# Optimization experiments

Measured on AMD Instinct MI355X. Metric: run time of the kernel, lower is better.

The kernel has to match this reference:

```python
import math
import jax, jax.numpy as jnp
import numpy as np

HEADS = 8


def setup_inputs() -> dict:
    key = jax.random.key(0)
    k1, k2, k3 = jax.random.split(key, 3)
    bs, C, H, Wd = 16, 512, 32, 32
    x = jax.random.normal(k1, (bs, C, H, Wd), dtype=jnp.float32)
    pos_enc = jax.random.normal(k2, (bs, C, H, Wd), dtype=jnp.float32)
    # 1x1 conv: weight [3C, C], bias [3C]
    W = jax.random.normal(k3, (3 * C, C), dtype=jnp.float32) * (1.0 / math.sqrt(C))
    b = jnp.zeros((3 * C,), dtype=jnp.float32)
    return {"x": x, "pos_enc": pos_enc, "W": W, "b": b}


def reference(x, pos_enc, W, b):
    x = x + pos_enc
    bs, C, H, Wd = x.shape
    heads = HEADS
    dim = C // heads
    N = H * Wd
    # 1x1 conv == channel matmul
    c = jnp.einsum('oc,bchw->bohw', W, x) + b[None, :, None, None]
    c = c.reshape(bs, 3, heads, dim, N)
    q = c[:, 0]  # [bs, heads, dim, N]
    k = c[:, 1]
    v = c[:, 2]
    scale = 1.0 / math.sqrt(dim)
    attn = jnp.einsum('bhdn,bhdm->bhnm', q, k) * scale  # [bs, heads, N, N]
    attn = jax.nn.softmax(attn, axis=-1)
    out = jnp.einsum('bhdm,bhnm->bhdn', v, attn)  # [bs, heads, dim, N]
    return x + out.reshape(bs, C, H, Wd)
```

## Files before the change

### kernel.cpp

```cpp
#include <hip/hip_runtime.h>
#include <stdint.h>


typedef __attribute__((ext_vector_type(4))) float f32x4;
typedef __attribute__((ext_vector_type(8))) __bf16 bf16x8;
typedef __attribute__((ext_vector_type(8))) short short8;
typedef __attribute__((ext_vector_type(4))) short short4v;

#define DEVINL static __device__ __forceinline__

DEVINL unsigned short f2bf(float f) {
  unsigned u = __builtin_bit_cast(unsigned, f);
  u += 0x7FFFu + ((u >> 16) & 1u);
  return (unsigned short)(u >> 16);
}

DEVINL void gload16(const void* g, const void* lds) {
  __builtin_amdgcn_global_load_lds(
      (const __attribute__((address_space(1))) unsigned int*)(uintptr_t)g,
      (__attribute__((address_space(3))) unsigned int*)(uintptr_t)lds, 16, 0, 0);
}

template <int CTRL>
DEVINL float dppmax(float x) {
  int yi = __builtin_amdgcn_update_dpp(0, __builtin_bit_cast(int, x), CTRL, 0xF, 0xF, true);
  return fmaxf(x, __builtin_bit_cast(float, yi));
}
DEVINL float rowmax16(float x) {
  x = dppmax<0xB1>(x);
  x = dppmax<0x4E>(x);
  x = dppmax<0x141>(x);
  x = dppmax<0x140>(x);
  return x;
}

__global__ __launch_bounds__(256) void k_conv(const float* __restrict__ Wf,
                                              unsigned short* __restrict__ wbo) {
  const int i = (blockIdx.x * 256 + threadIdx.x) * 4;
  const f32x4 v = *(const f32x4*)(Wf + i);
  short4v t;
  t[0] = (short)f2bf(v[0]); t[1] = (short)f2bf(v[1]);
  t[2] = (short)f2bf(v[2]); t[3] = (short)f2bf(v[3]);
  *(short4v*)(wbo + i) = t;
}

__global__ __launch_bounds__(256) void k_addt(const float* __restrict__ x,
                                              const float* __restrict__ pe,
                                              float* __restrict__ out,
                                              unsigned short* __restrict__ st) {
  __shared__ unsigned short T[64][64];
  const int b = blockIdx.z, ct = blockIdx.y, nt = blockIdx.x;
  const int tid = threadIdx.x;
  const int cl = tid >> 4, n4 = (tid & 15) * 4;
  const size_t base = ((size_t)b * 512 + ct * 64) * 1024 + nt * 64;
#pragma unroll
  for (int i = 0; i < 4; ++i) {
    const int c = cl + i * 16;
    const size_t idx = base + (size_t)c * 1024 + n4;
    const f32x4 xv = *(const f32x4*)(x + idx);
    const f32x4 pv = *(const f32x4*)(pe + idx);
    const f32x4 s = xv + pv;
    *(f32x4*)(out + idx) = s;
    short4v t;
    t[0] = (short)f2bf(s[0]); t[1] = (short)f2bf(s[1]);
    t[2] = (short)f2bf(s[2]); t[3] = (short)f2bf(s[3]);
    *(short4v*)&T[c][n4] = t;
  }
  __syncthreads();
  const int nl = tid >> 2, cq = tid & 3;
  short8 v0, v1;
#pragma unroll
  for (int j = 0; j < 8; ++j) {
    v0[j] = (short)T[cq * 16 + j][nl];
    v1[j] = (short)T[cq * 16 + 8 + j][nl];
  }
  const size_t so = ((size_t)b * 1024 + nt * 64 + nl) * 512 + ct * 64 + cq * 16;
  *(short8*)(st + so) = v0;
  *(short8*)(st + so + 8) = v1;
}

__global__ __launch_bounds__(256, 2) void k_gemm(const unsigned short* __restrict__ st,
                                                 const unsigned short* __restrict__ wb,
                                                 const float* __restrict__ bias,
                                                 unsigned short* __restrict__ qb,
                                                 unsigned short* __restrict__ kb,
                                                 unsigned short* __restrict__ vb) {
  const int b = blockIdx.z;
  const int mode = (blockIdx.y >= 8);
  const int tile_m = (mode ? (blockIdx.y - 8) : blockIdx.y) * 128;
  const int tile_n = blockIdx.x * 128;
  const unsigned short* Ag;
  const unsigned short* Bg;
  if (!mode) {
    Ag = st + (size_t)b * 524288 + (size_t)tile_m * 512;
    Bg = wb + (size_t)tile_n * 512;
  } else {
    Ag = wb + (size_t)(1024 + tile_m) * 512;
    Bg = st + (size_t)b * 524288 + (size_t)tile_n * 512;
  }
  __shared__ unsigned short As[4096];
  __shared__ unsigned short Bs[4096];
  const int tid = threadIdx.x, lane = tid & 63, w = tid >> 6;
  const int wrow = w >> 1, wcol = w & 1, lr = lane & 15, g = lane >> 4;
  f32x4 acc[4][4] = {};
  for (int kt = 0; kt < 16; ++kt) {
    __syncthreads();
#pragma unroll
    for (int j = 0; j < 2; ++j) {
      const int D = j * 4096 + w * 1024 + lane * 16;
      const int row = D >> 6, off = D & 63;
      gload16((const char*)Ag + (size_t)row * 1024 + kt * 64 + off,
              (const char*)As + j * 4096 + w * 1024);
      gload16((const char*)Bg + (size_t)row * 1024 + kt * 64 + off,
              (const char*)Bs + j * 4096 + w * 1024);
    }
    __syncthreads();
    bf16x8 a[4], bb[4];
#pragma unroll
    for (int i = 0; i < 4; ++i) {
      a[i]  = *(const bf16x8*)(As + (wrow * 64 + i * 16 + lr) * 32 + g * 8);
      bb[i] = *(const bf16x8*)(Bs + (wcol * 64 + i * 16 + lr) * 32 + g * 8);
    }
#pragma unroll
    for (int i = 0; i < 4; ++i)
#pragma unroll
      for (int jj = 0; jj < 4; ++jj)
        acc[i][jj] = __builtin_amdgcn_mfma_f32_16x16x32_bf16(a[i], bb[jj], acc[i][jj], 0, 0, 0);
  }
  if (!mode) {
#pragma unroll
    for (int jj = 0; jj < 4; ++jj) {
      const int o = tile_n + wcol * 64 + jj * 16 + lr;
      const float bv = bias[o];
      unsigned short* dst = (o < 512) ? qb : kb;
      const size_t rowbase = ((size_t)b * 8 + ((o >> 6) & 7)) * 1024;
      const int d = o & 63;
#pragma unroll
      for (int i = 0; i < 4; ++i) {
        const int n0 = tile_m + wrow * 64 + i * 16 + g * 4;
#pragma unroll
        for (int r = 0; r < 4; ++r)
          dst[(rowbase + n0 + r) * 64 + d] = f2bf(acc[i][jj][r] + bv);
      }
    }
  } else {
#pragma unroll
    for (int i = 0; i < 4; ++i) {
#pragma unroll
      for (int r = 0; r < 4; ++r) {
        const int oh = tile_m + wrow * 64 + i * 16 + g * 4 + r;
        const float bv = bias[1024 + oh];
        const size_t rb = (((size_t)b * 8 + (oh >> 6)) * 64 + (oh & 63)) * 1024;
#pragma unroll
        for (int jj = 0; jj < 4; ++jj) {
          const int n = tile_n + wcol * 64 + jj * 16 + lr;
          vb[rb + n] = f2bf(acc[i][jj][r] + bv);
        }
      }
    }
  }
}

__global__ __launch_bounds__(256, 2) void k_attn(const unsigned short* __restrict__ qb,
                                                 const unsigned short* __restrict__ kb,
                                                 const unsigned short* __restrict__ vb,
                                                 float* __restrict__ out) {
  __shared__ __align__(16) char smem[64 * 132 * 4];
  unsigned short* Ks = (unsigned short*)smem;
  unsigned short* Vs = (unsigned short*)(smem + 8192);
  char* Ps = smem + 16384;
  float* Os = (float*)smem;

  const int qt = blockIdx.x, bh = blockIdx.y;
  const int tid = threadIdx.x, lane = tid & 63, w = tid >> 6;
  const int lr = lane & 15, g = lane >> 4;
  const float F = 0.18033688011112042f;

  const unsigned short* qrow = qb + ((size_t)bh * 1024 + qt * 128 + w * 32) * 64;
  bf16x8 qf[2][2];
#pragma unroll
  for (int ai = 0; ai < 2; ++ai)
#pragma unroll
    for (int ks = 0; ks < 2; ++ks)
      qf[ai][ks] = *(const bf16x8*)(qrow + (ai * 16 + lr) * 64 + ks * 32 + g * 8);

  f32x4 Oacc[2][4] = {};
  float mrow[2][4], lrow[2][4];
#pragma unroll
  for (int ai = 0; ai < 2; ++ai)
#pragma unroll
    for (int r = 0; r < 4; ++r) { mrow[ai][r] = -__builtin_inff(); lrow[ai][r] = 0.f; }

  bf16x8 ones;
#pragma unroll
  for (int j = 0; j < 8; ++j) ones[j] = (__bf16)1.0f;

  const char* kbase = (const char*)(kb + (size_t)bh * 65536);
  const char* vbase = (const char*)(vb + (size_t)bh * 65536);

  for (int mt = 0; mt < 16; ++mt) {
    __syncthreads();
#pragma unroll
    for (int j = 0; j < 2; ++j) {
      const int D = j * 4096 + w * 1024 + lane * 16;
      const int row = D >> 7, ch = (D >> 4) & 7;
      const int sw = (ch ^ (row & 7)) * 16;
      gload16(kbase + (size_t)(mt * 64 + row) * 128 + sw, (const char*)Ks + j * 4096 + w * 1024);
      gload16(vbase + (size_t)row * 2048 + mt * 128 + sw, (const char*)Vs + j * 4096 + w * 1024);
    }
    __syncthreads();

    f32x4 s[2][4] = {};
#pragma unroll
    for (int ks = 0; ks < 2; ++ks) {
      bf16x8 kf[4];
#pragma unroll
      for (int ct = 0; ct < 4; ++ct)
        kf[ct] = *(const bf16x8*)((const char*)Ks + (ct * 16 + lr) * 128 +
                                  ((ks * 64 + g * 16) ^ ((lr & 7) << 4)));
#pragma unroll
      for (int ai = 0; ai < 2; ++ai)
#pragma unroll
        for (int ct = 0; ct < 4; ++ct)
          s[ai][ct] = __builtin_amdgcn_mfma_f32_16x16x32_bf16(qf[ai][ks], kf[ct], s[ai][ct], 0, 0, 0);
    }

    float alpha[2][4];
#pragma unroll
    for (int ai = 0; ai < 2; ++ai) {
#pragma unroll
      for (int r = 0; r < 4; ++r) {
        float tm = fmaxf(fmaxf(s[ai][0][r], s[ai][1][r]), fmaxf(s[ai][2][r], s[ai][3][r]));
        tm = rowmax16(tm);
        const float mn = fmaxf(mrow[ai][r], tm);
        alpha[ai][r] = __builtin_amdgcn_exp2f((mrow[ai][r] - mn) * F);
        mrow[ai][r] = mn;
        const int prow = ai * 16 + g * 4 + r;
#pragma unroll
        for (int ct = 0; ct < 4; ++ct) {
          const float p = __builtin_amdgcn_exp2f((s[ai][ct][r] - mn) * F);
          *(unsigned short*)(Ps + w * 4096 + prow * 128 +
                             ((ct * 32 + lr * 2) ^ ((prow & 7) << 4))) = f2bf(p);
        }
#pragma unroll
        for (int dt = 0; dt < 4; ++dt) Oacc[ai][dt][r] *= alpha[ai][r];
      }
    }

    f32x4 sacc[2] = {};
#pragma unroll
    for (int ks2 = 0; ks2 < 2; ++ks2) {
      bf16x8 pa[2];
#pragma unroll
      for (int ai = 0; ai < 2; ++ai) {
        pa[ai] = *(const bf16x8*)(Ps + w * 4096 + (ai * 16 + lr) * 128 +
                                  ((ks2 * 64 + g * 16) ^ ((lr & 7) << 4)));
        sacc[ai] = __builtin_amdgcn_mfma_f32_16x16x32_bf16(pa[ai], ones, sacc[ai], 0, 0, 0);
      }
#pragma unroll
      for (int dt = 0; dt < 4; ++dt) {
        const bf16x8 vf = *(const bf16x8*)((const char*)Vs + (dt * 16 + lr) * 128 +
                                           ((ks2 * 64 + g * 16) ^ ((lr & 7) << 4)));
#pragma unroll
        for (int ai = 0; ai < 2; ++ai)
          Oacc[ai][dt] = __builtin_amdgcn_mfma_f32_16x16x32_bf16(pa[ai], vf, Oacc[ai][dt], 0, 0, 0);
      }
    }
#pragma unroll
    for (int ai = 0; ai < 2; ++ai)
#pragma unroll
      for (int r = 0; r < 4; ++r)
        lrow[ai][r] = lrow[ai][r] * alpha[ai][r] + sacc[ai][r];
  }

  __syncthreads();
#pragma unroll
  for (int ai = 0; ai < 2; ++ai) {
#pragma unroll
    for (int r = 0; r < 4; ++r) {
      const float inv = 1.0f / lrow[ai][r];
#pragma unroll
      for (int dt = 0; dt < 4; ++dt)
        Os[(dt * 16 + lr) * 132 + (w * 32 + ai * 16 + g * 4 + r)] = Oacc[ai][dt][r] * inv;
    }
  }
  __syncthreads();
  const int d = tid >> 2, nq = tid & 3;
  float* orow = out + ((size_t)bh * 64 + d) * 1024 + qt * 128;
#pragma unroll
  for (int j = 0; j < 8; ++j) {
    const int n = nq * 32 + j * 4;
    const f32x4 ov = *(const f32x4*)(Os + d * 132 + n);
    const f32x4 cur = *(const f32x4*)(orow + n);
    *(f32x4*)(orow + n) = cur + ov;
  }
}

extern "C" void kernel_launch(void* const* d_in, const int* in_sizes, int n_in,
                              void* d_out, int out_size, void* d_ws, size_t ws_size,
                              hipStream_t stream) {
  const float* x    = (const float*)d_in[0];
  const float* pe   = (const float*)d_in[1];
  const float* W    = (const float*)d_in[2];
  const float* bias = (const float*)d_in[3];
  float* out = (float*)d_out;
  char* ws = (char*)d_ws;
  unsigned short* wb = (unsigned short*)(ws);
  unsigned short* st = (unsigned short*)(ws + ((size_t)2 << 20));
  unsigned short* qb = (unsigned short*)(ws + ((size_t)18 << 20));
  unsigned short* kb = (unsigned short*)(ws + ((size_t)34 << 20));
  unsigned short* vb = (unsigned short*)(ws + ((size_t)50 << 20));

  k_conv<<<dim3(768), dim3(256), 0, stream>>>(W, wb);
  k_addt<<<dim3(16, 8, 16), dim3(256), 0, stream>>>(x, pe, out, st);
  k_gemm<<<dim3(8, 12, 16), dim3(256), 0, stream>>>(st, wb, bias, qb, kb, vb);
  k_attn<<<dim3(8, 128), dim3(256), 0, stream>>>(qb, kb, vb, out);
}
```

Measured before the change: 244.6 us.

## Rewrite attention kernel with 32x32 MFMA, double-buffered K/V, and register-resident P

Rebuilds the flash-attention kernel around 32x32x16 MFMA, computing S transposed so each lane holds one query column. P now stays in registers, packed to bf16 and swapped across lane halves, instead of round-tripping through LDS. K/V tiles are double-buffered, so the next tile's load overlaps compute and one barrier per iteration goes away. The running max is updated lazily, rescaling only when it grows by more than a threshold. It also raises occupancy to 4 blocks per SM, remaps blocks so the 8 query tiles of one head are spread across XCDs, and writes output directly without LDS staging. Risks include register pressure at the higher occupancy, lazy-rescale precision, and uncoalesced strided output writes.

```diff
diff --git a/kernel.cpp b/kernel.cpp
--- a/kernel.cpp
+++ b/kernel.cpp
@@ -3,9 +3,11 @@
 
 
 typedef __attribute__((ext_vector_type(4))) float f32x4;
+typedef __attribute__((ext_vector_type(16))) float f32x16;
 typedef __attribute__((ext_vector_type(8))) __bf16 bf16x8;
 typedef __attribute__((ext_vector_type(8))) short short8;
 typedef __attribute__((ext_vector_type(4))) short short4v;
+typedef __attribute__((ext_vector_type(4))) int int4v;
 
 #define DEVINL static __device__ __forceinline__
 
@@ -21,17 +23,10 @@
       (__attribute__((address_space(3))) unsigned int*)(uintptr_t)lds, 16, 0, 0);
 }
 
-template <int CTRL>
-DEVINL float dppmax(float x) {
-  int yi = __builtin_amdgcn_update_dpp(0, __builtin_bit_cast(int, x), CTRL, 0xF, 0xF, true);
-  return fmaxf(x, __builtin_bit_cast(float, yi));
-}
-DEVINL float rowmax16(float x) {
-  x = dppmax<0xB1>(x);
-  x = dppmax<0x4E>(x);
-  x = dppmax<0x141>(x);
-  x = dppmax<0x140>(x);
-  return x;
+DEVINL int cvtpk(float lo, float hi) {
+  int d;
+  asm("v_cvt_pk_bf16_f32 %0, %1, %2" : "=v"(d) : "v"(lo), "v"(hi));
+  return d;
 }
 
 __global__ __launch_bounds__(256) void k_conv(const float* __restrict__ Wf,
@@ -161,138 +156,138 @@
   }
 }
 
-__global__ __launch_bounds__(256, 2) void k_attn(const unsigned short* __restrict__ qb,
+__global__ __launch_bounds__(256, 4) void k_attn(const unsigned short* __restrict__ qb,
                                                  const unsigned short* __restrict__ kb,
                                                  const unsigned short* __restrict__ vb,
                                                  float* __restrict__ out) {
-  __shared__ __align__(16) char smem[64 * 132 * 4];
-  unsigned short* Ks = (unsigned short*)smem;
-  unsigned short* Vs = (unsigned short*)(smem + 8192);
-  char* Ps = smem + 16384;
-  float* Os = (float*)smem;
-
-  const int qt = blockIdx.x, bh = blockIdx.y;
+  __shared__ __align__(16) char smem[32768];
+
+  const int f = blockIdx.x;
+  const int bh = (f & 7) * 16 + ((f >> 3) & 15);
+  const int qt = f >> 7;
+
   const int tid = threadIdx.x, lane = tid & 63, w = tid >> 6;
-  const int lr = lane & 15, g = lane >> 4;
+  const int ln = lane & 31, hf = lane >> 5;
   const float F = 0.18033688011112042f;
 
-  const unsigned short* qrow = qb + ((size_t)bh * 1024 + qt * 128 + w * 32) * 64;
-  bf16x8 qf[2][2];
-#pragma unroll
-  for (int ai = 0; ai < 2; ++ai)
-#pragma unroll
-    for (int ks = 0; ks < 2; ++ks)
-      qf[ai][ks] = *(const bf16x8*)(qrow + (ai * 16 + lr) * 64 + ks * 32 + g * 8);
-
-  f32x4 Oacc[2][4] = {};
-  float mrow[2][4], lrow[2][4];
-#pragma unroll
-  for (int ai = 0; ai < 2; ++ai)
-#pragma unroll
-    for (int r = 0; r < 4; ++r) { mrow[ai][r] = -__builtin_inff(); lrow[ai][r] = 0.f; }
-
-  bf16x8 ones;
-#pragma unroll
-  for (int j = 0; j < 8; ++j) ones[j] = (__bf16)1.0f;
-
-  const char* kbase = (const char*)(kb + (size_t)bh * 65536);
-  const char* vbase = (const char*)(vb + (size_t)bh * 65536);
-
+  const char* kbase = (const char*)kb + (size_t)bh * 131072;
+  const char* vbase = (const char*)vb + (size_t)bh * 131072;
+
+  const char* qrow = (const char*)qb + ((size_t)bh * 1024 + qt * 128 + w * 32 + ln) * 128;
+  bf16x8 qf[4];
+#pragma unroll
+  for (int c = 0; c < 4; ++c) qf[c] = *(const bf16x8*)(qrow + c * 32 + hf * 16);
+
+  f32x16 O0 = {}, O1 = {};
+  float mF = -__builtin_inff(), lsum = 0.f;
+
+#define STAGE(mt_, buf_)                                                          \
+  {                                                                               \
+    char* Kd = smem + (buf_) * 8192 + w * 1024;                                   \
+    char* Vd = smem + 16384 + (buf_) * 8192 + w * 1024;                           \
+    _Pragma("unroll") for (int j = 0; j < 2; ++j) {                               \
+      const int D = j * 4096 + w * 1024 + lane * 16;                              \
+      const int row = D >> 7, ch = (D >> 4) & 7;                                  \
+      const int sw = (ch ^ (row & 7)) * 16;                                       \
+      gload16(kbase + (size_t)((mt_) * 64 + row) * 128 + sw, Kd + j * 4096);      \
+      gload16(vbase + (size_t)row * 2048 + (mt_) * 128 + sw, Vd + j * 4096);      \
+    }                                                                             \
+  }
+
+  STAGE(0, 0);
+  __syncthreads();
+  int buf = 0;
   for (int mt = 0; mt < 16; ++mt) {
+    if (mt < 15) STAGE(mt + 1, buf ^ 1);
+    const char* Kc = smem + buf * 8192;
+    const char* Vc = smem + 16384 + buf * 8192;
+
+    f32x16 s0 = {}, s1 = {};
+#pragma unroll
+    for (int c = 0; c < 4; ++c) {
+      const int cb = ((c * 2 + hf) ^ (ln & 7)) * 16;
+      const bf16x8 k0 = *(const bf16x8*)(Kc + ln * 128 + cb);
+      s0 = __builtin_amdgcn_mfma_f32_32x32x16_bf16(k0, qf[c], s0, 0, 0, 0);
+      const bf16x8 k1 = *(const bf16x8*)(Kc + (32 + ln) * 128 + cb);
+      s1 = __builtin_amdgcn_mfma_f32_32x32x16_bf16(k1, qf[c], s1, 0, 0, 0);
+    }
+
+    float t = fmaxf(s0[0], s1[0]);
+#pragma unroll
+    for (int r = 1; r < 16; ++r) t = fmaxf(t, fmaxf(s0[r], s1[r]));
+    t = fmaxf(t, __shfl_xor(t, 32));
+    const float tF = t * F;
+    if (!__all(tF <= mF + 8.f)) {
+      const float mN = fmaxf(mF, tF);
+      const float al = __builtin_amdgcn_exp2f(mF - mN);
+#pragma unroll
+      for (int r = 0; r < 16; ++r) { O0[r] *= al; O1[r] *= al; }
+      lsum *= al;
+      mF = mN;
+    }
+
+#pragma unroll
+    for (int r = 0; r < 16; ++r) s0[r] = __builtin_amdgcn_exp2f(fmaf(s0[r], F, -mF));
+#pragma unroll
+    for (int r = 0; r < 16; ++r) s1[r] = __builtin_amdgcn_exp2f(fmaf(s1[r], F, -mF));
+
+    {
+      const f32x16 ps = s0 + s1;
+      float a0 = (ps[0] + ps[1]) + (ps[2] + ps[3]);
+      float a1 = (ps[4] + ps[5]) + (ps[6] + ps[7]);
+      float a2 = (ps[8] + ps[9]) + (ps[10] + ps[11]);
+      float a3 = (ps[12] + ps[13]) + (ps[14] + ps[15]);
+      float sm = (a0 + a1) + (a2 + a3);
+      lsum += sm + __shfl_xor(sm, 32);
+    }
+
+    int c0[8], c1[8];
+#pragma unroll
+    for (int j = 0; j < 8; ++j) {
+      c0[j] = cvtpk(s0[2 * j], s0[2 * j + 1]);
+      c1[j] = cvtpk(s1[2 * j], s1[2 * j + 1]);
+    }
+    int pw[4][4];
+#pragma unroll
+    for (int half = 0; half < 2; ++half) {
+      const int* cc = half ? c1 : c0;
+#pragma unroll
+      for (int q = 0; q < 2; ++q) {
+        const int b4 = q * 4, ch = half * 2 + q;
+        const int p0 = __shfl_xor(cc[b4 + 0], 32);
+        const int p1 = __shfl_xor(cc[b4 + 1], 32);
+        const int p2 = __shfl_xor(cc[b4 + 2], 32);
+        const int p3 = __shfl_xor(cc[b4 + 3], 32);
+        pw[ch][0] = hf ? p2 : cc[b4 + 0];
+        pw[ch][1] = hf ? p3 : cc[b4 + 1];
+        pw[ch][2] = hf ? cc[b4 + 2] : p0;
+        pw[ch][3] = hf ? cc[b4 + 3] : p1;
+      }
+    }
+
+#pragma unroll
+    for (int c = 0; c < 4; ++c) {
+      const int4v t4 = {pw[c][0], pw[c][1], pw[c][2], pw[c][3]};
+      const bf16x8 pb = __builtin_bit_cast(bf16x8, t4);
+      const int cb = ((c * 2 + hf) ^ (ln & 7)) * 16;
+      const bf16x8 v0 = *(const bf16x8*)(Vc + ln * 128 + cb);
+      O0 = __builtin_amdgcn_mfma_f32_32x32x16_bf16(v0, pb, O0, 0, 0, 0);
+      const bf16x8 v1 = *(const bf16x8*)(Vc + (32 + ln) * 128 + cb);
+      O1 = __builtin_amdgcn_mfma_f32_32x32x16_bf16(v1, pb, O1, 0, 0, 0);
+    }
+
     __syncthreads();
-#pragma unroll
-    for (int j = 0; j < 2; ++j) {
-      const int D = j * 4096 + w * 1024 + lane * 16;
-      const int row = D >> 7, ch = (D >> 4) & 7;
-      const int sw = (ch ^ (row & 7)) * 16;
-      gload16(kbase + (size_t)(mt * 64 + row) * 128 + sw, (const char*)Ks + j * 4096 + w * 1024);
-      gload16(vbase + (size_t)row * 2048 + mt * 128 + sw, (const char*)Vs + j * 4096 + w * 1024);
-    }
-    __syncthreads();
-
-    f32x4 s[2][4] = {};
-#pragma unroll
-    for (int ks = 0; ks < 2; ++ks) {
-      bf16x8 kf[4];
-#pragma unroll
-      for (int ct = 0; ct < 4; ++ct)
-        kf[ct] = *(const bf16x8*)((const char*)Ks + (ct * 16 + lr) * 128 +
-                                  ((ks * 64 + g * 16) ^ ((lr & 7) << 4)));
-#pragma unroll
-      for (int ai = 0; ai < 2; ++ai)
-#pragma unroll
-        for (int ct = 0; ct < 4; ++ct)
-          s[ai][ct] = __builtin_amdgcn_mfma_f32_16x16x32_bf16(qf[ai][ks], kf[ct], s[ai][ct], 0, 0, 0);
-    }
-
-    float alpha[2][4];
-#pragma unroll
-    for (int ai = 0; ai < 2; ++ai) {
-#pragma unroll
-      for (int r = 0; r < 4; ++r) {
-        float tm = fmaxf(fmaxf(s[ai][0][r], s[ai][1][r]), fmaxf(s[ai][2][r], s[ai][3][r]));
-        tm = rowmax16(tm);
-        const float mn = fmaxf(mrow[ai][r], tm);
-        alpha[ai][r] = __builtin_amdgcn_exp2f((mrow[ai][r] - mn) * F);
-        mrow[ai][r] = mn;
-        const int prow = ai * 16 + g * 4 + r;
-#pragma unroll
-        for (int ct = 0; ct < 4; ++ct) {
-          const float p = __builtin_amdgcn_exp2f((s[ai][ct][r] - mn) * F);
-          *(unsigned short*)(Ps + w * 4096 + prow * 128 +
-                             ((ct * 32 + lr * 2) ^ ((prow & 7) << 4))) = f2bf(p);
-        }
-#pragma unroll
-        for (int dt = 0; dt < 4; ++dt) Oacc[ai][dt][r] *= alpha[ai][r];
-      }
-    }
-
-    f32x4 sacc[2] = {};
-#pragma unroll
-    for (int ks2 = 0; ks2 < 2; ++ks2) {
-      bf16x8 pa[2];
-#pragma unroll
-      for (int ai = 0; ai < 2; ++ai) {
-        pa[ai] = *(const bf16x8*)(Ps + w * 4096 + (ai * 16 + lr) * 128 +
-                                  ((ks2 * 64 + g * 16) ^ ((lr & 7) << 4)));
-        sacc[ai] = __builtin_amdgcn_mfma_f32_16x16x32_bf16(pa[ai], ones, sacc[ai], 0, 0, 0);
-      }
-#pragma unroll
-      for (int dt = 0; dt < 4; ++dt) {
-        const bf16x8 vf = *(const bf16x8*)((const char*)Vs + (dt * 16 + lr) * 128 +
-                                           ((ks2 * 64 + g * 16) ^ ((lr & 7) << 4)));
-#pragma unroll
-        for (int ai = 0; ai < 2; ++ai)
-          Oacc[ai][dt] = __builtin_amdgcn_mfma_f32_16x16x32_bf16(pa[ai], vf, Oacc[ai][dt], 0, 0, 0);
-      }
-    }
-#pragma unroll
-    for (int ai = 0; ai < 2; ++ai)
-#pragma unroll
-      for (int r = 0; r < 4; ++r)
-        lrow[ai][r] = lrow[ai][r] * alpha[ai][r] + sacc[ai][r];
-  }
-
-  __syncthreads();
-#pragma unroll
-  for (int ai = 0; ai < 2; ++ai) {
-#pragma unroll
-    for (int r = 0; r < 4; ++r) {
-      const float inv = 1.0f / lrow[ai][r];
-#pragma unroll
-      for (int dt = 0; dt < 4; ++dt)
-        Os[(dt * 16 + lr) * 132 + (w * 32 + ai * 16 + g * 4 + r)] = Oacc[ai][dt][r] * inv;
-    }
-  }
-  __syncthreads();
-  const int d = tid >> 2, nq = tid & 3;
-  float* orow = out + ((size_t)bh * 64 + d) * 1024 + qt * 128;
-#pragma unroll
-  for (int j = 0; j < 8; ++j) {
-    const int n = nq * 32 + j * 4;
-    const f32x4 ov = *(const f32x4*)(Os + d * 132 + n);
-    const f32x4 cur = *(const f32x4*)(orow + n);
-    *(f32x4*)(orow + n) = cur + ov;
+    buf ^= 1;
+  }
+#undef STAGE
+
+  const float inv = 1.0f / lsum;
+  float* obase = out + ((size_t)bh * 64) * 1024 + qt * 128 + w * 32 + ln;
+#pragma unroll
+  for (int r = 0; r < 16; ++r) {
+    const int d0 = (r & 3) + 8 * (r >> 2) + 4 * hf;
+    obase[(size_t)d0 * 1024] += O0[r] * inv;
+    obase[(size_t)(d0 + 32) * 1024] += O1[r] * inv;
   }
 }
 
@@ -314,5 +309,5 @@
   k_conv<<<dim3(768), dim3(256), 0, stream>>>(W, wb);
   k_addt<<<dim3(16, 8, 16), dim3(256), 0, stream>>>(x, pe, out, st);
   k_gemm<<<dim3(8, 12, 16), dim3(256), 0, stream>>>(st, wb, bias, qb, kb, vb);
-  k_attn<<<dim3(8, 128), dim3(256), 0, stream>>>(qb, kb, vb, out);
-}
+  k_attn<<<dim3(1024), dim3(256), 0, stream>>>(qb, kb, vb, out);
+}
```

New measurement: 215.1 us. 12.1% less time.
